# Kernel optimization log

Measured on AMD Instinct MI355X. Metric: run time of the kernel, lower is better.

## Reference

```python
import jax, jax.numpy as jnp
import numpy as np

B, S, K, N, GROUP = 4, 8, 4096, 11008, 128
NUM_GROUPS = K // GROUP  # 32


def setup_inputs() -> dict:
    key = jax.random.key(0)
    k1, k2, k3 = jax.random.split(key, 3)
    x = jax.random.normal(k1, (B, S, K), dtype=jnp.float16)
    # packed int4 weights: each byte holds two nibbles (low nibble = even k, high = odd k)
    weight_packed = jax.random.randint(k2, (N, K // 2), 0, 256, dtype=jnp.int32)
    # scales: abs(randn)*0.1 in fp16, as in the torch module
    scales = (jnp.abs(jax.random.normal(k3, (N, NUM_GROUPS), dtype=jnp.float16)) * jnp.float16(0.1))
    return {"x": x, "weight_packed": weight_packed, "scales": scales}


def _dequant(weight_packed, scales, Kd):
    # unpack: low nibble -> even index k, high nibble -> odd index k+1
    n = weight_packed.shape[0]
    low = weight_packed & 0xF
    high = (weight_packed >> 4) & 0xF
    w = jnp.stack([low, high], axis=-1).reshape(n, Kd)  # [N, K] int in [0,16)
    g = Kd // scales.shape[1]
    # group-wise dequant: scale * (w - 8), scale applied in fp32 (matches fp32-accum kernel)
    wq = (w.astype(jnp.float32) - 8.0).reshape(n, scales.shape[1], g)
    wdeq = wq * scales.astype(jnp.float32)[:, :, None]
    return wdeq.reshape(n, Kd)  # [N, K] fp32


def reference(x, weight_packed, scales):
    b, s, kd = x.shape
    wdeq = _dequant(weight_packed, scales, kd)           # [N, K]
    x2 = x.reshape(-1, kd).astype(jnp.float32)           # [M, K], fp32 accumulation
    out = jnp.einsum('mk,nk->mn', x2, wdeq)              # [M, N]
    return out.astype(jnp.float16).reshape(b, s, -1)
```

## Files before the change

### kernel.cpp

```cpp
#include <hip/hip_runtime.h>

#define M 32
#define N 11008
#define K 4096
#define NGROUPS 32
#define BN 16
#define WAVES 8
#define KW 512

typedef _Float16 half8 __attribute__((ext_vector_type(8)));
typedef _Float16 half4 __attribute__((ext_vector_type(4)));
typedef float floatx4 __attribute__((ext_vector_type(4)));

__global__ __launch_bounds__(512) void xcvt_kernel(
    const float* __restrict__ x, _Float16* __restrict__ xf)
{
    int i = (blockIdx.x * 512 + threadIdx.x) * 4;
    float4 v = *(const float4*)(x + i);
    half4 h;
    h[0] = (_Float16)v.x; h[1] = (_Float16)v.y;
    h[2] = (_Float16)v.z; h[3] = (_Float16)v.w;
    *(half4*)(xf + i) = h;
}

__global__ __launch_bounds__(512, 6) void int4_gemm_kernel(
    const _Float16* __restrict__ x,
    const int* __restrict__ wp,
    const float* __restrict__ scales,
    float* __restrict__ out)
{
    __shared__ float red[WAVES * M * BN];

    const int t    = threadIdx.x;
    const int lane = t & 63;
    const int w    = t >> 6;
    const int n0   = blockIdx.x * BN;
    const int row  = lane & 15;
    const int quad = lane >> 4;

    const int* wrow        = wp + (long)(n0 + row) * (K / 2) + w * (KW / 2) + quad * 4;
    const float* srow      = scales + (n0 + row) * NGROUPS + w * (KW / 128);
    const _Float16* xr0    = x + row * K + w * KW + quad * 8;
    const _Float16* xr1    = xr0 + 16 * K;

    floatx4 acc0 = {0.f, 0.f, 0.f, 0.f};
    floatx4 acc1 = {0.f, 0.f, 0.f, 0.f};

    #pragma unroll
    for (int g = 0; g < KW / 128; ++g) {
        const float s = srow[g];
        floatx4 t0 = {0.f, 0.f, 0.f, 0.f};
        floatx4 t1 = {0.f, 0.f, 0.f, 0.f};
        #pragma unroll
        for (int kk = 0; kk < 4; ++kk) {
            const int koff = g * 128 + kk * 32;
            int4 b4 = *(const int4*)(wrow + (koff >> 1));
            int arr[4] = {b4.x, b4.y, b4.z, b4.w};
            half8 bfrag;
            #pragma unroll
            for (int j = 0; j < 4; ++j) {
                bfrag[2 * j]     = (_Float16)((arr[j] & 15) - 8);
                bfrag[2 * j + 1] = (_Float16)(((arr[j] >> 4) & 15) - 8);
            }
            half8 a0 = *(const half8*)(xr0 + koff);
            half8 a1 = *(const half8*)(xr1 + koff);
            t0 = __builtin_amdgcn_mfma_f32_16x16x32_f16(a0, bfrag, t0, 0, 0, 0);
            t1 = __builtin_amdgcn_mfma_f32_16x16x32_f16(a1, bfrag, t1, 0, 0, 0);
        }
        #pragma unroll
        for (int r = 0; r < 4; ++r) {
            acc0[r] += s * t0[r];
            acc1[r] += s * t1[r];
        }
    }

    #pragma unroll
    for (int r = 0; r < 4; ++r) {
        red[w * (M * BN) + (quad * 4 + r) * BN + row]      = acc0[r];
        red[w * (M * BN) + (quad * 4 + r + 16) * BN + row] = acc1[r];
    }
    __syncthreads();

    {
        float sum = 0.f;
        #pragma unroll
        for (int i = 0; i < WAVES; ++i) sum += red[i * (M * BN) + t];
        int m = t >> 4;
        int n = t & 15;
        out[m * N + n0 + n] = sum;
    }
}

extern "C" void kernel_launch(void* const* d_in, const int* in_sizes, int n_in,
                              void* d_out, int out_size, void* d_ws, size_t ws_size,
                              hipStream_t stream) {
    const float* x      = (const float*)d_in[0];
    const int* wp       = (const int*)d_in[1];
    const float* scales = (const float*)d_in[2];
    float* out          = (float*)d_out;
    _Float16* xf16      = (_Float16*)d_ws;

    xcvt_kernel<<<dim3((M * K) / (512 * 4)), 512, 0, stream>>>(x, xf16);
    int4_gemm_kernel<<<dim3(N / BN), 512, 0, stream>>>(xf16, wp, scales, out);
}
```

Baseline: 158.8 us.

## Split K across blocks, stage tiles via global_load_lds, use magic-number int4 dequant

```diff
diff --git a/kernel.cpp b/kernel.cpp
--- a/kernel.cpp
+++ b/kernel.cpp
@@ -5,12 +5,23 @@
 #define K 4096
 #define NGROUPS 32
 #define BN 16
-#define WAVES 8
-#define KW 512
+#define KSPLIT 4
+#define KRANGE (K / KSPLIT)
+#define BK 256
+#define NCHUNK (KRANGE / BK)
 
 typedef _Float16 half8 __attribute__((ext_vector_type(8)));
 typedef _Float16 half4 __attribute__((ext_vector_type(4)));
 typedef float floatx4 __attribute__((ext_vector_type(4)));
+
+#define WPAIR 260
+#define XPAIR 520
+
+__device__ inline void gll16(const void* g, void* l) {
+    __builtin_amdgcn_global_load_lds(
+        (const __attribute__((address_space(1))) unsigned int*)g,
+        (__attribute__((address_space(3))) unsigned int*)l, 16, 0, 0);
+}
 
 __global__ __launch_bounds__(512) void xcvt_kernel(
     const float* __restrict__ x, _Float16* __restrict__ xf)
@@ -23,47 +34,71 @@
     *(half4*)(xf + i) = h;
 }
 
-__global__ __launch_bounds__(512, 6) void int4_gemm_kernel(
-    const _Float16* __restrict__ x,
+__global__ __launch_bounds__(256) void int4_gemm_kernel(
+    const _Float16* __restrict__ xf,
     const int* __restrict__ wp,
     const float* __restrict__ scales,
     float* __restrict__ out)
 {
-    __shared__ float red[WAVES * M * BN];
+    __shared__ int wsh[8 * WPAIR];
+    __shared__ _Float16 xs[16 * XPAIR];
 
     const int t    = threadIdx.x;
     const int lane = t & 63;
     const int w    = t >> 6;
     const int n0   = blockIdx.x * BN;
+    const int ks   = blockIdx.y;
     const int row  = lane & 15;
     const int quad = lane >> 4;
-
-    const int* wrow        = wp + (long)(n0 + row) * (K / 2) + w * (KW / 2) + quad * 4;
-    const float* srow      = scales + (n0 + row) * NGROUPS + w * (KW / 128);
-    const _Float16* xr0    = x + row * K + w * KW + quad * 8;
-    const _Float16* xr1    = xr0 + 16 * K;
 
     floatx4 acc0 = {0.f, 0.f, 0.f, 0.f};
     floatx4 acc1 = {0.f, 0.f, 0.f, 0.f};
 
-    #pragma unroll
-    for (int g = 0; g < KW / 128; ++g) {
-        const float s = srow[g];
+    const half8 c1032 = (half8)(_Float16)1032.0f;
+
+    for (int c = 0; c < NCHUNK; ++c) {
+        const int kc = ks * KRANGE + c * BK;
+
+        #pragma unroll
+        for (int i = 0; i < 2; ++i) {
+            int p = w * 2 + i;
+            int r = 2 * p + (lane >> 5);
+            const int* g = wp + (long)(n0 + r) * (K / 2) + (kc >> 1) + (lane & 31) * 4;
+            gll16(g, &wsh[p * WPAIR]);
+        }
+        #pragma unroll
+        for (int i = 0; i < 4; ++i) {
+            int p = w * 4 + i;
+            int m = 2 * p + (lane >> 5);
+            const _Float16* g = xf + m * K + kc + (lane & 31) * 8;
+            gll16(g, &xs[p * XPAIR]);
+        }
+        __syncthreads();
+
+        const float s = scales[(n0 + row) * NGROUPS + (kc >> 7) + (w >> 1)];
         floatx4 t0 = {0.f, 0.f, 0.f, 0.f};
         floatx4 t1 = {0.f, 0.f, 0.f, 0.f};
         #pragma unroll
-        for (int kk = 0; kk < 4; ++kk) {
-            const int koff = g * 128 + kk * 32;
-            int4 b4 = *(const int4*)(wrow + (koff >> 1));
-            int arr[4] = {b4.x, b4.y, b4.z, b4.w};
-            half8 bfrag;
-            #pragma unroll
-            for (int j = 0; j < 4; ++j) {
-                bfrag[2 * j]     = (_Float16)((arr[j] & 15) - 8);
-                bfrag[2 * j + 1] = (_Float16)(((arr[j] >> 4) & 15) - 8);
+        for (int kk = 0; kk < 2; ++kk) {
+            const int kl = w * 64 + kk * 32;
+            int4 wv = *(const int4*)&wsh[(row >> 1) * WPAIR + (row & 1) * 128 + (kl >> 1) + quad * 4];
+            uint4 uw;
+            {
+                unsigned int b;
+                b = (unsigned int)wv.x;
+                uw.x = ((b | (b << 12)) & 0x000F000Fu) | 0x64006400u;
+                b = (unsigned int)wv.y;
+                uw.y = ((b | (b << 12)) & 0x000F000Fu) | 0x64006400u;
+                b = (unsigned int)wv.z;
+                uw.z = ((b | (b << 12)) & 0x000F000Fu) | 0x64006400u;
+                b = (unsigned int)wv.w;
+                uw.w = ((b | (b << 12)) & 0x000F000Fu) | 0x64006400u;
             }
-            half8 a0 = *(const half8*)(xr0 + koff);
-            half8 a1 = *(const half8*)(xr1 + koff);
+            half8 bfrag = __builtin_bit_cast(half8, uw) - c1032;
+
+            int x0 = (row >> 1) * XPAIR + (row & 1) * 256 + kl + quad * 8;
+            half8 a0 = *(const half8*)&xs[x0];
+            half8 a1 = *(const half8*)&xs[x0 + 8 * XPAIR];
             t0 = __builtin_amdgcn_mfma_f32_16x16x32_f16(a0, bfrag, t0, 0, 0, 0);
             t1 = __builtin_amdgcn_mfma_f32_16x16x32_f16(a1, bfrag, t1, 0, 0, 0);
         }
@@ -72,22 +107,23 @@
             acc0[r] += s * t0[r];
             acc1[r] += s * t1[r];
         }
+        __syncthreads();
     }
 
+    float* red = (float*)xs;
     #pragma unroll
     for (int r = 0; r < 4; ++r) {
-        red[w * (M * BN) + (quad * 4 + r) * BN + row]      = acc0[r];
-        red[w * (M * BN) + (quad * 4 + r + 16) * BN + row] = acc1[r];
+        red[w * 512 + (quad * 4 + r) * 16 + row]      = acc0[r];
+        red[w * 512 + (quad * 4 + r + 16) * 16 + row] = acc1[r];
     }
     __syncthreads();
-
-    {
-        float sum = 0.f;
-        #pragma unroll
-        for (int i = 0; i < WAVES; ++i) sum += red[i * (M * BN) + t];
-        int m = t >> 4;
-        int n = t & 15;
-        out[m * N + n0 + n] = sum;
+    #pragma unroll
+    for (int i = 0; i < 2; ++i) {
+        int o = t + 256 * i;
+        float sum = red[o] + red[512 + o] + red[1024 + o] + red[1536 + o];
+        int m = o >> 4;
+        int n = o & 15;
+        atomicAdd(&out[m * N + n0 + n], sum);
     }
 }
 
@@ -100,6 +136,7 @@
     float* out          = (float*)d_out;
     _Float16* xf16      = (_Float16*)d_ws;
 
+    hipMemsetAsync(out, 0, (size_t)M * N * sizeof(float), stream);
     xcvt_kernel<<<dim3((M * K) / (512 * 4)), 512, 0, stream>>>(x, xf16);
-    int4_gemm_kernel<<<dim3(N / BN), 512, 0, stream>>>(xf16, wp, scales, out);
+    int4_gemm_kernel<<<dim3(N / BN, KSPLIT), 256, 0, stream>>>(xf16, wp, scales, out);
 }
```

Measured after the change: 141.8 us. 1.12x faster.
